# Optimization experiments

Hardware: AMD Instinct MI355X
Metric: run time of the kernel (lower is better)

The kernel has to match this reference:

```python
import jax, jax.numpy as jnp
import numpy as np
import math

LOCAL_WINDOW = 256  # matches init_kwargs local_window

B, H, S, DK = 1, 16, 2048, 64


def setup_inputs() -> dict:
    key = jax.random.key(0)
    kq, kk, kv = jax.random.split(key, 3)
    return {
        "q": jax.random.normal(kq, (B, H, S, DK), dtype=jnp.float32),
        "k": jax.random.normal(kk, (B, H, S, DK), dtype=jnp.float32),
        "v": jax.random.normal(kv, (B, H, S, DK), dtype=jnp.float32),
        "layer_idx": 1,
        "training": 0,
    }


def _make_mask(seq_len: int, layer_idx: int) -> jnp.ndarray:
    i = jnp.arange(seq_len)[:, None]
    j = jnp.arange(seq_len)[None, :]
    causal = j <= i
    if layer_idx % 2 == 0:
        return causal  # full causal mask
    # local banded mask: causal AND within local_window
    return causal & ((i - j) < LOCAL_WINDOW)


def reference(q, k, v, layer_idx, training):
    # past=None path: no KV-cache concat; present = (k, v)
    dk = q.shape[-1]
    # scores: [B, H, S, S]
    scores = jnp.einsum("bhqd,bhkd->bhqk", q, k) / math.sqrt(dk)
    seq_len = scores.shape[-1]
    mask = _make_mask(seq_len, layer_idx)  # [S, S], broadcast over B, H
    scores = jnp.where(mask, scores, jnp.float32(-1e9))
    weights = jax.nn.softmax(scores, axis=-1)
    # training=0 -> no dropout (deterministic reference)
    context = jnp.einsum("bhqk,bhkd->bhqd", weights, v)
    return (context, k, v)  # (context, present)
```

## Files before the change

### kernel.cpp

```cpp
#include <hip/hip_runtime.h>

#define S_DIM 2048
#define H_DIM 16
#define DK_DIM 64
#define TQ 64
#define TK 64
#define KSP 72
#define VTP 72
#define PSP 72
#define WINDOW 256

typedef short short8 __attribute__((ext_vector_type(8)));
typedef float floatx4 __attribute__((ext_vector_type(4)));

static __device__ __forceinline__ short f2bf(float f) {
    unsigned u = __builtin_bit_cast(unsigned, f);
    u = (u + 0x7fffu + ((u >> 16) & 1u)) >> 16;
    return (short)u;
}

__global__ __launch_bounds__(256, 2)
void attn_kernel(const float* __restrict__ qg,
                 const float* __restrict__ kg,
                 const float* __restrict__ vg,
                 const int* __restrict__ layer_idx_p,
                 float* __restrict__ outc,
                 float* __restrict__ outk,
                 float* __restrict__ outv)
{
    __shared__ __align__(16) short Ks[TK * KSP];
    __shared__ __align__(16) short Vts[DK_DIM * VTP];
    __shared__ __align__(16) short Ps[4 * 16 * PSP];

    const int bid  = blockIdx.x;
    const int xcd  = bid & 7;
    const int slot = bid >> 3;
    const int h    = xcd * 2 + (slot >> 5);
    const int q0   = (slot & 31) * TQ;

    const int tid  = threadIdx.x;
    const int w    = tid >> 6;
    const int lane = tid & 63;
    const int quad = lane >> 4;
    const int l16  = lane & 15;

    const int li  = layer_idx_p[0];
    const int wnd = (li & 1) ? WINDOW : S_DIM;

    {
        const size_t base = ((size_t)(h * S_DIM + q0)) * DK_DIM;
        const floatx4* ks4 = (const floatx4*)(kg + base);
        const floatx4* vs4 = (const floatx4*)(vg + base);
        floatx4* ok4 = (floatx4*)(outk + base);
        floatx4* ov4 = (floatx4*)(outv + base);
        #pragma unroll
        for (int i = 0; i < 4; ++i) {
            int f = tid + i * 256;
            ok4[f] = ks4[f];
            ov4[f] = vs4[f];
        }
    }

    const int qrow = q0 + w * 16 + l16;
    const size_t qbase = ((size_t)(h * S_DIM + qrow)) * DK_DIM;
    short8 qf0, qf1;
    {
        floatx4 a0 = *(const floatx4*)(qg + qbase + quad * 8);
        floatx4 a1 = *(const floatx4*)(qg + qbase + quad * 8 + 4);
        floatx4 b0 = *(const floatx4*)(qg + qbase + 32 + quad * 8);
        floatx4 b1 = *(const floatx4*)(qg + qbase + 32 + quad * 8 + 4);
        #pragma unroll
        for (int j = 0; j < 4; ++j) {
            qf0[j]     = f2bf(a0[j] * 0.125f);
            qf0[j + 4] = f2bf(a1[j] * 0.125f);
            qf1[j]     = f2bf(b0[j] * 0.125f);
            qf1[j + 4] = f2bf(b1[j] * 0.125f);
        }
    }

    floatx4 Oacc[4];
    floatx4 Lacc = (floatx4){0.f, 0.f, 0.f, 0.f};
    #pragma unroll
    for (int dt = 0; dt < 4; ++dt) Oacc[dt] = (floatx4){0.f, 0.f, 0.f, 0.f};

    short8 ones;
    #pragma unroll
    for (int j = 0; j < 8; ++j) ones[j] = (short)0x3F80;

    int lo = q0 - (wnd - 1); if (lo < 0) lo = 0;
    const int kb0  = lo & ~(TK - 1);
    const int kend = q0 + TQ - 1;

    floatx4 kraw[2][2];
    float   vraw[2][8];
    const int krow[2] = { (tid * 8) >> 6, ((tid + 256) * 8) >> 6 };
    const int kcol[2] = { (tid * 8) & 63, ((tid + 256) * 8) & 63 };
    const int vd  [2] = { tid & 63, (tid + 256) & 63 };
    const int vkg [2] = { tid >> 6, (tid + 256) >> 6 };

    auto preload = [&](int kb) {
        #pragma unroll
        for (int it = 0; it < 2; ++it) {
            const float* p = kg + ((size_t)(h * S_DIM + kb + krow[it])) * DK_DIM + kcol[it];
            kraw[it][0] = *(const floatx4*)p;
            kraw[it][1] = *(const floatx4*)(p + 4);
            #pragma unroll
            for (int j = 0; j < 8; ++j)
                vraw[it][j] = vg[((size_t)(h * S_DIM + kb + vkg[it] * 8 + j)) * DK_DIM + vd[it]];
        }
    };
    auto commit = [&]() {
        #pragma unroll
        for (int it = 0; it < 2; ++it) {
            short8 val;
            #pragma unroll
            for (int j = 0; j < 4; ++j) {
                val[j]     = f2bf(kraw[it][0][j]);
                val[j + 4] = f2bf(kraw[it][1][j]);
            }
            *(short8*)(&Ks[krow[it] * KSP + kcol[it]]) = val;
            short8 tmp;
            #pragma unroll
            for (int j = 0; j < 8; ++j) tmp[j] = f2bf(vraw[it][j]);
            *(short8*)(&Vts[vd[it] * VTP + vkg[it] * 8]) = tmp;
        }
    };

    preload(kb0);

    for (int kb = kb0; kb <= kend; kb += TK) {
        commit();
        __syncthreads();
        if (kb + TK <= kend) preload(kb + TK);

        #pragma unroll
        for (int ct = 0; ct < 4; ++ct) {
            floatx4 acc = (floatx4){0.f, 0.f, 0.f, 0.f};
            short8 b0 = *(const short8*)(&Ks[(ct * 16 + l16) * KSP +      quad * 8]);
            acc = __builtin_amdgcn_mfma_f32_16x16x32_bf16(qf0, b0, acc, 0, 0, 0);
            short8 b1 = *(const short8*)(&Ks[(ct * 16 + l16) * KSP + 32 + quad * 8]);
            acc = __builtin_amdgcn_mfma_f32_16x16x32_bf16(qf1, b1, acc, 0, 0, 0);
            const int col = kb + ct * 16 + l16;
            #pragma unroll
            for (int r = 0; r < 4; ++r) {
                int row = q0 + w * 16 + quad * 4 + r;
                bool valid = (col <= row) && ((row - col) < wnd);
                float pv = valid ? __expf(acc[r]) : 0.f;
                Ps[(w * 16 + quad * 4 + r) * PSP + ct * 16 + l16] = f2bf(pv);
            }
        }

        #pragma unroll
        for (int ks = 0; ks < 2; ++ks) {
            short8 af = *(const short8*)(&Ps[(w * 16 + l16) * PSP + ks * 32 + quad * 8]);
            Lacc = __builtin_amdgcn_mfma_f32_16x16x32_bf16(af, ones, Lacc, 0, 0, 0);
            #pragma unroll
            for (int dt = 0; dt < 4; ++dt) {
                short8 bf = *(const short8*)(&Vts[(dt * 16 + l16) * VTP + ks * 32 + quad * 8]);
                Oacc[dt] = __builtin_amdgcn_mfma_f32_16x16x32_bf16(af, bf, Oacc[dt], 0, 0, 0);
            }
        }
        __syncthreads();
    }

    #pragma unroll
    for (int r = 0; r < 4; ++r) {
        float inv = 1.0f / Lacc[r];
        int row = q0 + w * 16 + quad * 4 + r;
        size_t obase = ((size_t)(h * S_DIM + row)) * DK_DIM;
        #pragma unroll
        for (int dt = 0; dt < 4; ++dt)
            outc[obase + dt * 16 + l16] = Oacc[dt][r] * inv;
    }
}

extern "C" void kernel_launch(void* const* d_in, const int* in_sizes, int n_in,
                              void* d_out, int out_size, void* d_ws, size_t ws_size,
                              hipStream_t stream) {
    const float* q  = (const float*)d_in[0];
    const float* k  = (const float*)d_in[1];
    const float* v  = (const float*)d_in[2];
    const int* li   = (const int*)d_in[3];
    float* out      = (float*)d_out;

    const int nctx = in_sizes[0];
    float* outk = out + nctx;
    float* outv = out + nctx + in_sizes[1];

    const int grid_attn = H_DIM * (S_DIM / TQ);
    attn_kernel<<<grid_attn, 256, 0, stream>>>(q, k, v, li, out, outk, outv);
}
```

Measured before the change: 95.10 us.

## Double-buffer K/V LDS tiles, skip fully masked subtiles, use exp2

K and V tiles in LDS are now double-buffered, so the loop needs one barrier per iteration instead of two, and the next tile's global load is issued two tiles ahead. Each wave skips QK and PV MFMAs for 16-column subtiles that lie entirely outside its causal or window band, and drops per-element mask checks on subtiles that are fully inside it. The softmax scale is folded with log2(e) into Q so the hardware exp2 can replace expf. This costs twice the K/V LDS footprint, which may lower occupancy, and the early preload is reordered ahead of the K/V copy-out.

```diff
diff --git a/kernel.cpp b/kernel.cpp
--- a/kernel.cpp
+++ b/kernel.cpp
@@ -19,6 +19,12 @@
     return (short)u;
 }
 
+static __device__ __forceinline__ void lds_barrier() {
+    asm volatile("s_waitcnt lgkmcnt(0)" ::: "memory");
+    __builtin_amdgcn_s_barrier();
+    asm volatile("" ::: "memory");
+}
+
 __global__ __launch_bounds__(256, 2)
 void attn_kernel(const float* __restrict__ qg,
                  const float* __restrict__ kg,
@@ -28,9 +34,9 @@
                  float* __restrict__ outk,
                  float* __restrict__ outv)
 {
-    __shared__ __align__(16) short Ks[TK * KSP];
-    __shared__ __align__(16) short Vts[DK_DIM * VTP];
-    __shared__ __align__(16) short Ps[4 * 16 * PSP];
+    __shared__ __align__(16) short Ks [2 * TK * KSP];
+    __shared__ __align__(16) short Vts[2 * DK_DIM * VTP];
+    __shared__ __align__(16) short Ps [4 * 16 * PSP];
 
     const int bid  = blockIdx.x;
     const int xcd  = bid & 7;
@@ -46,6 +52,49 @@
 
     const int li  = layer_idx_p[0];
     const int wnd = (li & 1) ? WINDOW : S_DIM;
+
+    int lo = q0 - (wnd - 1); if (lo < 0) lo = 0;
+    const int kb0  = lo & ~(TK - 1);
+    const int kend = q0 + TQ - 1;
+
+    floatx4 kraw[2][2];
+    float   vraw[2][8];
+    const int krow[2] = { (tid * 8) >> 6, ((tid + 256) * 8) >> 6 };
+    const int kcol[2] = { (tid * 8) & 63, ((tid + 256) * 8) & 63 };
+    const int vd_ [2] = { tid & 63, (tid + 256) & 63 };
+    const int vkg [2] = { tid >> 6, (tid + 256) >> 6 };
+
+    auto preload = [&](int kb) {
+        #pragma unroll
+        for (int it = 0; it < 2; ++it) {
+            const float* p = kg + ((size_t)(h * S_DIM + kb + krow[it])) * DK_DIM + kcol[it];
+            kraw[it][0] = *(const floatx4*)p;
+            kraw[it][1] = *(const floatx4*)(p + 4);
+            #pragma unroll
+            for (int j = 0; j < 8; ++j)
+                vraw[it][j] = vg[((size_t)(h * S_DIM + kb + vkg[it] * 8 + j)) * DK_DIM + vd_[it]];
+        }
+    };
+    auto commit = [&](int nb) {
+        short* Kd = &Ks [nb * (TK * KSP)];
+        short* Vd = &Vts[nb * (DK_DIM * VTP)];
+        #pragma unroll
+        for (int it = 0; it < 2; ++it) {
+            short8 val;
+            #pragma unroll
+            for (int j = 0; j < 4; ++j) {
+                val[j]     = f2bf(kraw[it][0][j]);
+                val[j + 4] = f2bf(kraw[it][1][j]);
+            }
+            *(short8*)(&Kd[krow[it] * KSP + kcol[it]]) = val;
+            short8 tmp;
+            #pragma unroll
+            for (int j = 0; j < 8; ++j) tmp[j] = f2bf(vraw[it][j]);
+            *(short8*)(&Vd[vd_[it] * VTP + vkg[it] * 8]) = tmp;
+        }
+    };
+
+    preload(kb0);
 
     {
         const size_t base = ((size_t)(h * S_DIM + q0)) * DK_DIM;
@@ -65,16 +114,17 @@
     const size_t qbase = ((size_t)(h * S_DIM + qrow)) * DK_DIM;
     short8 qf0, qf1;
     {
+        const float qs = 0.125f * 1.4426950408889634f;
         floatx4 a0 = *(const floatx4*)(qg + qbase + quad * 8);
         floatx4 a1 = *(const floatx4*)(qg + qbase + quad * 8 + 4);
         floatx4 b0 = *(const floatx4*)(qg + qbase + 32 + quad * 8);
         floatx4 b1 = *(const floatx4*)(qg + qbase + 32 + quad * 8 + 4);
         #pragma unroll
         for (int j = 0; j < 4; ++j) {
-            qf0[j]     = f2bf(a0[j] * 0.125f);
-            qf0[j + 4] = f2bf(a1[j] * 0.125f);
-            qf1[j]     = f2bf(b0[j] * 0.125f);
-            qf1[j + 4] = f2bf(b1[j] * 0.125f);
+            qf0[j]     = f2bf(a0[j] * qs);
+            qf0[j + 4] = f2bf(a1[j] * qs);
+            qf1[j]     = f2bf(b0[j] * qs);
+            qf1[j + 4] = f2bf(b1[j] * qs);
         }
     }
 
@@ -87,86 +137,72 @@
     #pragma unroll
     for (int j = 0; j < 8; ++j) ones[j] = (short)0x3F80;
 
-    int lo = q0 - (wnd - 1); if (lo < 0) lo = 0;
-    const int kb0  = lo & ~(TK - 1);
-    const int kend = q0 + TQ - 1;
-
-    floatx4 kraw[2][2];
-    float   vraw[2][8];
-    const int krow[2] = { (tid * 8) >> 6, ((tid + 256) * 8) >> 6 };
-    const int kcol[2] = { (tid * 8) & 63, ((tid + 256) * 8) & 63 };
-    const int vd  [2] = { tid & 63, (tid + 256) & 63 };
-    const int vkg [2] = { tid >> 6, (tid + 256) >> 6 };
-
-    auto preload = [&](int kb) {
-        #pragma unroll
-        for (int it = 0; it < 2; ++it) {
-            const float* p = kg + ((size_t)(h * S_DIM + kb + krow[it])) * DK_DIM + kcol[it];
-            kraw[it][0] = *(const floatx4*)p;
-            kraw[it][1] = *(const floatx4*)(p + 4);
-            #pragma unroll
-            for (int j = 0; j < 8; ++j)
-                vraw[it][j] = vg[((size_t)(h * S_DIM + kb + vkg[it] * 8 + j)) * DK_DIM + vd[it]];
-        }
-    };
-    auto commit = [&]() {
-        #pragma unroll
-        for (int it = 0; it < 2; ++it) {
-            short8 val;
-            #pragma unroll
-            for (int j = 0; j < 4; ++j) {
-                val[j]     = f2bf(kraw[it][0][j]);
-                val[j + 4] = f2bf(kraw[it][1][j]);
-            }
-            *(short8*)(&Ks[krow[it] * KSP + kcol[it]]) = val;
-            short8 tmp;
-            #pragma unroll
-            for (int j = 0; j < 8; ++j) tmp[j] = f2bf(vraw[it][j]);
-            *(short8*)(&Vts[vd[it] * VTP + vkg[it] * 8]) = tmp;
-        }
-    };
-
-    preload(kb0);
-
+    commit(0);
+    if (kb0 + TK <= kend) preload(kb0 + TK);
+    lds_barrier();
+
+    int cur = 0;
+    const int rmin = q0 + w * 16;
     for (int kb = kb0; kb <= kend; kb += TK) {
-        commit();
-        __syncthreads();
-        if (kb + TK <= kend) preload(kb + TK);
+        const short* Kc = &Ks [cur * (TK * KSP)];
+        const short* Vc = &Vts[cur * (DK_DIM * VTP)];
 
         #pragma unroll
         for (int ct = 0; ct < 4; ++ct) {
+            const int colbase = kb + ct * 16;
+            if (colbase > rmin + 15 || rmin - (colbase + 15) >= wnd) {
+                #pragma unroll
+                for (int r = 0; r < 4; ++r)
+                    Ps[(w * 16 + quad * 4 + r) * PSP + ct * 16 + l16] = 0;
+                continue;
+            }
             floatx4 acc = (floatx4){0.f, 0.f, 0.f, 0.f};
-            short8 b0 = *(const short8*)(&Ks[(ct * 16 + l16) * KSP +      quad * 8]);
+            short8 b0 = *(const short8*)(&Kc[(ct * 16 + l16) * KSP +      quad * 8]);
             acc = __builtin_amdgcn_mfma_f32_16x16x32_bf16(qf0, b0, acc, 0, 0, 0);
-            short8 b1 = *(const short8*)(&Ks[(ct * 16 + l16) * KSP + 32 + quad * 8]);
+            short8 b1 = *(const short8*)(&Kc[(ct * 16 + l16) * KSP + 32 + quad * 8]);
             acc = __builtin_amdgcn_mfma_f32_16x16x32_bf16(qf1, b1, acc, 0, 0, 0);
-            const int col = kb + ct * 16 + l16;
-            #pragma unroll
-            for (int r = 0; r < 4; ++r) {
-                int row = q0 + w * 16 + quad * 4 + r;
-                bool valid = (col <= row) && ((row - col) < wnd);
-                float pv = valid ? __expf(acc[r]) : 0.f;
-                Ps[(w * 16 + quad * 4 + r) * PSP + ct * 16 + l16] = f2bf(pv);
+            if (colbase + 15 <= rmin && (rmin + 15 - colbase) < wnd) {
+                #pragma unroll
+                for (int r = 0; r < 4; ++r)
+                    Ps[(w * 16 + quad * 4 + r) * PSP + ct * 16 + l16] =
+                        f2bf(__builtin_amdgcn_exp2f(acc[r]));
+            } else {
+                const int col = colbase + l16;
+                #pragma unroll
+                for (int r = 0; r < 4; ++r) {
+                    int row = rmin + quad * 4 + r;
+                    bool valid = (col <= row) && ((row - col) < wnd);
+                    float pv = valid ? __builtin_amdgcn_exp2f(acc[r]) : 0.f;
+                    Ps[(w * 16 + quad * 4 + r) * PSP + ct * 16 + l16] = f2bf(pv);
+                }
             }
         }
 
         #pragma unroll
         for (int ks = 0; ks < 2; ++ks) {
+            const int cb = kb + ks * 32;
+            if (cb > rmin + 15 || rmin - (cb + 31) >= wnd) continue;
             short8 af = *(const short8*)(&Ps[(w * 16 + l16) * PSP + ks * 32 + quad * 8]);
             Lacc = __builtin_amdgcn_mfma_f32_16x16x32_bf16(af, ones, Lacc, 0, 0, 0);
             #pragma unroll
             for (int dt = 0; dt < 4; ++dt) {
-                short8 bf = *(const short8*)(&Vts[(dt * 16 + l16) * VTP + ks * 32 + quad * 8]);
+                short8 bf = *(const short8*)(&Vc[(dt * 16 + l16) * VTP + ks * 32 + quad * 8]);
                 Oacc[dt] = __builtin_amdgcn_mfma_f32_16x16x32_bf16(af, bf, Oacc[dt], 0, 0, 0);
             }
         }
-        __syncthreads();
+
+        if (kb + TK <= kend) {
+            commit(cur ^ 1);
+            if (kb + 2 * TK <= kend) preload(kb + 2 * TK);
+            lds_barrier();
+        }
+        cur ^= 1;
     }
 
     #pragma unroll
     for (int r = 0; r < 4; ++r) {
         float inv = 1.0f / Lacc[r];
-        int row = q0 + w * 16 + quad * 4 + r;
+        int row = rmin + quad * 4 + r;
         size_t obase = ((size_t)(h * S_DIM + row)) * DK_DIM;
         #pragma unroll
         for (int dt = 0; dt < 4; ++dt)
```

Measured after the change: 94.76 us. About the same (-0.4%).
